# Kernel optimization log

Measured on AMD Instinct MI355X. Metric: run time of the kernel, lower is better.

The kernel has to match this reference:

```python
import jax, jax.numpy as jnp
import numpy as np

N, E, G, F = 100000, 3200000, 256, 15
NEG_SLOPE = 0.2


def _lin(k, fi, fo):
    s = 1.0 / np.sqrt(fi)
    return jax.random.uniform(k, (fi, fo), jnp.float32, -s, s)


def _vec(k, n, fi):
    s = 1.0 / np.sqrt(fi)
    return jax.random.uniform(k, (n,), jnp.float32, -s, s)


def setup_inputs() -> dict:
    key = jax.random.key(0)
    ks = jax.random.split(key, 40)
    inp = {}
    inp["x"] = jax.random.normal(ks[0], (N, F), jnp.float32)
    inp["edge_index"] = jax.random.randint(ks[1], (2, E), 0, N, dtype=jnp.int32)
    inp["batch"] = jnp.sort(jax.random.randint(ks[2], (N,), 0, G, dtype=jnp.int32))
    inp["xA"] = jax.random.normal(ks[3], (G, 300), jnp.float32)
    i = 4
    for l in (1, 2, 3):
        inp[f"cW{l}"] = _lin(ks[i], F, F); i += 1
        inp[f"cas{l}"] = _vec(ks[i], F, F); i += 1
        inp[f"cad{l}"] = _vec(ks[i], F, F); i += 1
        inp[f"cb{l}"] = jnp.zeros((F,), jnp.float32)
        inp[f"fW{l}"] = _lin(ks[i], F, F); i += 1
        inp[f"fb{l}"] = _vec(ks[i], F, F); i += 1
    inp["m1W"] = _lin(ks[i], 90, 90); i += 1
    inp["m1b"] = _vec(ks[i], 90, 90); i += 1
    inp["aW1"] = _lin(ks[i], 300, 300); i += 1
    inp["ab1"] = _vec(ks[i], 300, 300); i += 1
    inp["aW2"] = _lin(ks[i], 300, 300); i += 1
    inp["ab2"] = _vec(ks[i], 300, 300); i += 1
    inp["aW3"] = _lin(ks[i], 300, 300); i += 1
    inp["ab3"] = _vec(ks[i], 300, 300); i += 1
    inp["aW4"] = _lin(ks[i], 300, 45); i += 1
    inp["ab4"] = _vec(ks[i], 45, 300); i += 1
    inp["m2W"] = _lin(ks[i], 90, 1); i += 1
    inp["m2b"] = _vec(ks[i], 1, 90); i += 1
    return inp


def _gat(x, src, dst, W, a_s, a_d, b):
    """PyG GATConv (heads=1, add_self_loops handled by caller via src/dst)."""
    h = x @ W                                        # [N, F]
    e = jax.nn.leaky_relu((h @ a_s)[src] + (h @ a_d)[dst], NEG_SLOPE)  # [E+N]
    mx = jax.ops.segment_max(e, dst, num_segments=N)
    ex = jnp.exp(e - mx[dst])
    den = jax.ops.segment_sum(ex, dst, num_segments=N)
    alpha = ex / (den[dst] + 1e-16)                   # segment softmax over dst
    out = jax.ops.segment_sum(h[src] * alpha[:, None], dst, num_segments=N)
    return out + b


def reference(x, edge_index, batch, xA,
              cW1, cas1, cad1, cb1, fW1, fb1,
              cW2, cas2, cad2, cb2, fW2, fb2,
              cW3, cas3, cad3, cb3, fW3, fb3,
              m1W, m1b, aW1, ab1, aW2, ab2, aW3, ab3, aW4, ab4,
              m2W, m2b):
    loop = jnp.arange(N, dtype=edge_index.dtype)      # self loops
    src = jnp.concatenate([edge_index[0], loop])
    dst = jnp.concatenate([edge_index[1], loop])

    h = _gat(x, src, dst, cW1, cas1, cad1, cb1)
    h = jax.nn.relu(h @ fW1 + fb1)
    h = _gat(h, src, dst, cW2, cas2, cad2, cb2)
    h = jax.nn.relu(h @ fW2 + fb2)
    h = _gat(h, src, dst, cW3, cas3, cad3, cb3)
    h = h @ fW3 + fb3

    s = jax.ops.segment_sum(h, batch, num_segments=G)
    mx = jax.ops.segment_max(h, batch, num_segments=G)
    cnt = jax.ops.segment_sum(jnp.ones((N, 1), h.dtype), batch, num_segments=G)
    mean = s / jnp.maximum(cnt, 1.0)
    pooled = jnp.concatenate([s, mx, mean], axis=1)   # [G, 45]

    a = jax.nn.relu(xA @ aW1 + ab1)
    a = jax.nn.relu(a @ aW2 + ab2)
    a = jax.nn.sigmoid(a @ aW3 + ab3)
    xann = a @ aW4 + ab4                              # [G, 45]

    z = jnp.concatenate([pooled, xann], axis=1)       # [G, 90]
    z = jax.nn.relu(z @ m1W + m1b)
    z = z @ m2W + m2b
    return jax.nn.sigmoid(z)
```

## Files before the change

### kernel.cpp

```cpp
#include <hip/hip_runtime.h>
#include <hip/hip_bf16.h>
#include <math.h>

#define FDIM 15
#define FPAD 16
#define NEG_SLOPE 0.2f
#define BSH 8
#define BWID 256
#define HB_GRID 256
#define HB_BLK 1024

typedef _Float16 half_t;

__device__ __forceinline__ float leaky(float e) {
  return fmaxf(NEG_SLOPE * e, e);
}

__global__ void k_zero(int* __restrict__ p, int n) {
  int i = blockIdx.x * blockDim.x + threadIdx.x;
  if (i < n) p[i] = 0;
}

__global__ void k_bhist(const int* __restrict__ dstI, int* __restrict__ bcnt,
                        int n_tot, int n_real, int NB) {
  __shared__ int hist[512];
  int tid = threadIdx.x;
  for (int i = tid; i < NB; i += blockDim.x) hist[i] = 0;
  __syncthreads();
  int stride = gridDim.x * blockDim.x;
  for (int i = blockIdx.x * blockDim.x + tid; i < n_tot; i += stride) {
    int d = (i < n_real) ? dstI[i] : (i - n_real);
    atomicAdd(&hist[d >> BSH], 1);
  }
  __syncthreads();
  for (int i = tid; i < NB; i += blockDim.x)
    if (hist[i]) atomicAdd(&bcnt[i], hist[i]);
}

__global__ void k_bscan(const int* __restrict__ bcnt, int* __restrict__ boff,
                        int* __restrict__ bcur, int* __restrict__ rowptr,
                        int NB, int N, int total) {
  __shared__ int s[512];
  int tid = threadIdx.x;
  int v = (tid < NB) ? bcnt[tid] : 0;
  s[tid] = v;
  __syncthreads();
  for (int off = 1; off < 512; off <<= 1) {
    int add = (tid >= off) ? s[tid - off] : 0;
    __syncthreads();
    s[tid] += add;
    __syncthreads();
  }
  if (tid < NB) { int e = s[tid] - v; boff[tid] = e; bcur[tid] = e; }
  if (tid == NB - 1) boff[NB] = s[tid];
  if (tid == 0) rowptr[N] = total;
}

__global__ void k_bpart(const int* __restrict__ srcI, const int* __restrict__ dstI,
                        int* __restrict__ bcur, int* __restrict__ bbuf,
                        int n_tot, int n_real, int NB) {
  __shared__ int hist[512];
  __shared__ int base[512];
  int tid = threadIdx.x;
  for (int i = tid; i < NB; i += blockDim.x) hist[i] = 0;
  __syncthreads();
  int stride = gridDim.x * blockDim.x;
  int g0 = blockIdx.x * blockDim.x + tid;
  for (int i = g0; i < n_tot; i += stride) {
    int d = (i < n_real) ? dstI[i] : (i - n_real);
    atomicAdd(&hist[d >> BSH], 1);
  }
  __syncthreads();
  for (int i = tid; i < NB; i += blockDim.x)
    base[i] = hist[i] ? atomicAdd(&bcur[i], hist[i]) : 0;
  __syncthreads();
  for (int i = tid; i < NB; i += blockDim.x) hist[i] = 0;
  __syncthreads();
  for (int i = g0; i < n_tot; i += stride) {
    int s, d;
    if (i < n_real) { s = srcI[i]; d = dstI[i]; }
    else { s = d = i - n_real; }
    int b = d >> BSH;
    int p = base[b] + atomicAdd(&hist[b], 1);
    bbuf[p] = (s << BSH) | (d & (BWID - 1));
  }
}

__global__ void k_bbuild(const int* __restrict__ boff, const int* __restrict__ bbuf,
                         int* __restrict__ rowptr, int* __restrict__ csr, int N) {
  __shared__ int hist[BWID];
  __shared__ int sc[BWID];
  int b = blockIdx.x;
  int tid = threadIdx.x;
  int base_dst = b << BSH;
  int nd = min(BWID, N - base_dst);
  int s0 = boff[b], s1 = boff[b + 1];
  if (tid < BWID) hist[tid] = 0;
  __syncthreads();
  for (int j = s0 + tid; j < s1; j += 512)
    atomicAdd(&hist[bbuf[j] & (BWID - 1)], 1);
  __syncthreads();
  int v = 0;
  if (tid < BWID) { v = hist[tid]; sc[tid] = v; }
  __syncthreads();
  for (int off = 1; off < BWID; off <<= 1) {
    int add = 0;
    if (tid < BWID && tid >= off) add = sc[tid - off];
    __syncthreads();
    if (tid < BWID) sc[tid] += add;
    __syncthreads();
  }
  if (tid < nd) rowptr[base_dst + tid] = s0 + sc[tid] - v;
  __syncthreads();
  if (tid < BWID) hist[tid] = sc[tid] - v;
  __syncthreads();
  for (int j = s0 + tid; j < s1; j += 512) {
    int e = bbuf[j];
    int dl = e & (BWID - 1);
    int p = s0 + atomicAdd(&hist[dl], 1);
    csr[p] = (e >> BSH) << 5;
  }
}

__global__ void k_transform(const float* __restrict__ in, int ld_in,
                            const float* __restrict__ W,
                            const float* __restrict__ a_s,
                            const float* __restrict__ a_d,
                            half_t* __restrict__ hp,
                            float* __restrict__ ad_,
                            int n_nodes) {
  __shared__ float Ws[FDIM * FDIM];
  __shared__ float asv[FDIM], adv[FDIM];
  int tid = threadIdx.x;
  if (tid < FDIM * FDIM) Ws[tid] = W[tid];
  if (tid < FDIM) { asv[tid] = a_s[tid]; adv[tid] = a_d[tid]; }
  __syncthreads();
  int n = blockIdx.x * blockDim.x + tid;
  if (n >= n_nodes) return;
  float xin[FDIM];
#pragma unroll
  for (int j = 0; j < FDIM; ++j) xin[j] = in[n * ld_in + j];
  float sa = 0.f, da = 0.f;
  half_t hrow[FPAD];
#pragma unroll
  for (int o = 0; o < FDIM; ++o) {
    float acc = 0.f;
#pragma unroll
    for (int k = 0; k < FDIM; ++k) acc += xin[k] * Ws[k * FDIM + o];
    hrow[o] = (half_t)acc;
    sa += acc * asv[o];
    da += acc * adv[o];
  }
  hrow[FDIM] = (half_t)sa;
  ad_[n] = da;
  float4 w0, w1;
  __builtin_memcpy(&w0, &hrow[0], 16);
  __builtin_memcpy(&w1, &hrow[8], 16);
  float4* dst = (float4*)(hp + (size_t)n * FPAD);
  dst[0] = w0;
  dst[1] = w1;
}

__device__ __forceinline__ void mlp_rider(int g, int tid, int nthreads,
                                          const float* __restrict__ mIn,
                                          const float* __restrict__ mW,
                                          const float* __restrict__ mB,
                                          float* __restrict__ mOut,
                                          int Nout, int mAct,
                                          float* mins) {
  for (int k = tid; k < 300; k += nthreads) mins[k] = mIn[(size_t)g * 300 + k];
  __syncthreads();
  int j1 = tid;
  int j2 = tid + nthreads;
  bool p1 = (j1 < Nout), p2 = (j2 < Nout);
  if (!p1) return;
  float a0 = 0.f, a1 = 0.f, a2 = 0.f, a3 = 0.f;
  float a4 = 0.f, a5 = 0.f, a6 = 0.f, a7 = 0.f;
  float b0 = 0.f, b1 = 0.f, b2 = 0.f, b3 = 0.f;
  float b4 = 0.f, b5 = 0.f, b6 = 0.f, b7 = 0.f;
  int k = 0;
  for (; k + 7 < 300; k += 8) {
    float i0 = mins[k],     i1 = mins[k + 1], i2 = mins[k + 2], i3 = mins[k + 3];
    float i4 = mins[k + 4], i5 = mins[k + 5], i6 = mins[k + 6], i7 = mins[k + 7];
    float w0 = mW[k * Nout + j1];
    float w1 = mW[(k + 1) * Nout + j1];
    float w2 = mW[(k + 2) * Nout + j1];
    float w3 = mW[(k + 3) * Nout + j1];
    float w4 = mW[(k + 4) * Nout + j1];
    float w5 = mW[(k + 5) * Nout + j1];
    float w6 = mW[(k + 6) * Nout + j1];
    float w7 = mW[(k + 7) * Nout + j1];
    a0 += i0 * w0; a1 += i1 * w1; a2 += i2 * w2; a3 += i3 * w3;
    a4 += i4 * w4; a5 += i5 * w5; a6 += i6 * w6; a7 += i7 * w7;
    if (p2) {
      float v0 = mW[k * Nout + j2];
      float v1 = mW[(k + 1) * Nout + j2];
      float v2 = mW[(k + 2) * Nout + j2];
      float v3 = mW[(k + 3) * Nout + j2];
      float v4 = mW[(k + 4) * Nout + j2];
      float v5 = mW[(k + 5) * Nout + j2];
      float v6 = mW[(k + 6) * Nout + j2];
      float v7 = mW[(k + 7) * Nout + j2];
      b0 += i0 * v0; b1 += i1 * v1; b2 += i2 * v2; b3 += i3 * v3;
      b4 += i4 * v4; b5 += i5 * v5; b6 += i6 * v6; b7 += i7 * v7;
    }
  }
  for (; k < 300; ++k) {
    float ik = mins[k];
    a0 += ik * mW[k * Nout + j1];
    if (p2) b0 += ik * mW[k * Nout + j2];
  }
  float r1 = mB[j1] + ((a0 + a1) + (a2 + a3)) + ((a4 + a5) + (a6 + a7));
  if (mAct == 1) r1 = fmaxf(r1, 0.f);
  else if (mAct == 2) r1 = 1.f / (1.f + expf(-r1));
  mOut[(size_t)g * Nout + j1] = r1;
  if (p2) {
    float r2 = mB[j2] + ((b0 + b1) + (b2 + b3)) + ((b4 + b5) + (b6 + b7));
    if (mAct == 1) r2 = fmaxf(r2, 0.f);
    else if (mAct == 2) r2 = 1.f / (1.f + expf(-r2));
    mOut[(size_t)g * Nout + j2] = r2;
  }
}

__global__ void k_gat(const int* __restrict__ rowptr, const int* __restrict__ csrB,
                      const half_t* __restrict__ hp, const float* __restrict__ ad_,
                      const float* __restrict__ cb, const float* __restrict__ fW,
                      const float* __restrict__ fb,
                      const float* __restrict__ nW, const float* __restrict__ nas,
                      const float* __restrict__ nad,
                      half_t* __restrict__ hp2, float* __restrict__ ad2,
                      float* __restrict__ fout,
                      const float* __restrict__ mIn, const float* __restrict__ mW,
                      const float* __restrict__ mB, float* __restrict__ mOut,
                      int mNout, int mAct, int mlpG,
                      int n_nodes, int do_relu, int fuse) {
  __shared__ float Ws[FDIM * FDIM];
  __shared__ float W2s[FDIM * FDIM];
  __shared__ float cbv[FDIM], fbv[FDIM], as2v[FDIM], ad2v[FDIM];
  __shared__ float aggT[16][16];
  __shared__ float outT[16][16];
  __shared__ float mins[304];
  int tid = threadIdx.x;

  if ((int)blockIdx.x < mlpG) {
    mlp_rider(blockIdx.x, tid, blockDim.x, mIn, mW, mB, mOut, mNout, mAct, mins);
    return;
  }

  if (tid < FDIM * FDIM) Ws[tid] = fW[tid];
  if (tid < FDIM) { cbv[tid] = cb[tid]; fbv[tid] = fb[tid]; }
  if (fuse) {
    if (tid < FDIM * FDIM) W2s[tid] = nW[tid];
    if (tid < FDIM) { as2v[tid] = nas[tid]; ad2v[tid] = nad[tid]; }
  }
  __syncthreads();
  int dl = tid >> 4;
  int f  = tid & 15;
  int e4 = f >> 2;
  int c  = f & 3;
  int d  = ((int)blockIdx.x - mlpG) * 16 + dl;
  float r0 = 0.f, r1 = 0.f, r2 = 0.f, r3 = 0.f;
  if (d < n_nodes) {
    int rs = rowptr[d], re = rowptr[d + 1];
    float adv = ad_[d];
    const char* hb = (const char*)hp;
    int co = c << 3;
    int srcl = f | 3;
    float acc0 = 0.f, acc1 = 0.f, acc2 = 0.f, acc3 = 0.f, den = 0.f;
    for (int j = rs; j < re; j += 8) {
      int i0 = j + e4;
      int i1 = i0 + 4;
      int o0 = csrB[i0 < re ? i0 : re - 1];
      int o1 = csrB[i1 < re ? i1 : re - 1];
      uint2 u0 = *(const uint2*)(hb + o0 + co);
      uint2 u1 = *(const uint2*)(hb + o1 + co);
      half_t h0[4], h1[4];
      __builtin_memcpy(h0, &u0, 8);
      __builtin_memcpy(h1, &u1, 8);
      float a0 = (float)h0[0], a1 = (float)h0[1], a2 = (float)h0[2], a3 = (float)h0[3];
      float b0 = (float)h1[0], b1 = (float)h1[1], b2 = (float)h1[2], b3 = (float)h1[3];
      float s0 = __shfl(a3, srcl, 16);
      float s1 = __shfl(b3, srcl, 16);
      float w0 = (i0 < re) ? __expf(leaky(s0 + adv)) : 0.f;
      float w1 = (i1 < re) ? __expf(leaky(s1 + adv)) : 0.f;
      den  += w0 + w1;
      acc0 += a0 * w0 + b0 * w1;
      acc1 += a1 * w0 + b1 * w1;
      acc2 += a2 * w0 + b2 * w1;
      acc3 += a3 * w0 + b3 * w1;
    }
    den  += __shfl_xor(den,  4, 16);
    acc0 += __shfl_xor(acc0, 4, 16);
    acc1 += __shfl_xor(acc1, 4, 16);
    acc2 += __shfl_xor(acc2, 4, 16);
    acc3 += __shfl_xor(acc3, 4, 16);
    den  += __shfl_xor(den,  8, 16);
    acc0 += __shfl_xor(acc0, 8, 16);
    acc1 += __shfl_xor(acc1, 8, 16);
    acc2 += __shfl_xor(acc2, 8, 16);
    acc3 += __shfl_xor(acc3, 8, 16);
    float inv = 1.f / (den + 1e-16f);
    r0 = acc0 * inv; r1 = acc1 * inv; r2 = acc2 * inv; r3 = acc3 * inv;
  }
  if (e4 == 0) {
    int base = c << 2;
    aggT[dl][base]     = r0 + cbv[base];
    aggT[dl][base + 1] = r1 + cbv[base + 1];
    aggT[dl][base + 2] = r2 + cbv[base + 2];
    aggT[dl][base + 3] = (base + 3 < FDIM) ? (r3 + cbv[base + 3]) : 0.f;
  }
  __syncthreads();
  int o = f;
  float ffn = 0.f;
  if (o < FDIM) {
    ffn = fbv[o];
#pragma unroll
    for (int k = 0; k < FDIM; ++k) ffn += aggT[dl][k] * Ws[k * FDIM + o];
    if (do_relu) ffn = fmaxf(ffn, 0.f);
  }
  if (!fuse) {
    if (d < n_nodes) fout[d * FPAD + o] = (o < FDIM) ? ffn : 0.f;
    return;
  }
  outT[dl][o] = ffn;
  __syncthreads();
  if (d < n_nodes) {
    float h2 = 0.f;
    if (o < FDIM) {
#pragma unroll
      for (int k = 0; k < FDIM; ++k) h2 += outT[dl][k] * W2s[k * FDIM + o];
    }
    float pa = (o < FDIM) ? h2 * as2v[o] : 0.f;
    float pd = (o < FDIM) ? h2 * ad2v[o] : 0.f;
#pragma unroll
    for (int k = 8; k; k >>= 1) {
      pa += __shfl_xor(pa, k, 16);
      pd += __shfl_xor(pd, k, 16);
    }
    hp2[(size_t)d * FPAD + o] = (half_t)((o < FDIM) ? h2 : pa);
    if (o == 0) ad2[d] = pd;
  }
}

__device__ __forceinline__ int lowerb(const int* __restrict__ a, int n, int key) {
  int lo = 0, hi = n;
  while (lo < hi) { int mid = (lo + hi) >> 1; if (a[mid] < key) lo = mid + 1; else hi = mid; }
  return lo;
}

__global__ void k_pool(const float* __restrict__ fout, const int* __restrict__ batch,
                       float* __restrict__ pooled,
                       const float* __restrict__ acts,
                       const float* __restrict__ aW4, const float* __restrict__ ab4,
                       float* __restrict__ xann,
                       int n_nodes, int Gn) {
  __shared__ float ss[256], sm[256];
  __shared__ float mins[304];
  int tid = threadIdx.x;
  if ((int)blockIdx.x < Gn) {
    mlp_rider(blockIdx.x, tid, blockDim.x, acts, aW4, ab4, xann, 45, 0, mins);
    return;
  }
  int g = blockIdx.x - Gn;
  int s = lowerb(batch, n_nodes, g);
  int e = lowerb(batch, n_nodes, g + 1);
  int f = tid & 15;
  float sum = 0.f, mx = -INFINITY;
  for (int n = s + (tid >> 4); n < e; n += 16) {
    float v = fout[n * FPAD + f];
    sum += v;
    mx = fmaxf(mx, v);
  }
  ss[tid] = sum; sm[tid] = mx;
  __syncthreads();
  for (int step = 128; step >= 16; step >>= 1) {
    if (tid < step) { ss[tid] += ss[tid + step]; sm[tid] = fmaxf(sm[tid], sm[tid + step]); }
    __syncthreads();
  }
  if (tid < FDIM) {
    float cnt = (float)(e - s);
    float sv = ss[tid];
    pooled[g * 45 + tid] = sv;
    pooled[g * 45 + 15 + tid] = sm[tid];
    pooled[g * 45 + 30 + tid] = sv / fmaxf(cnt, 1.f);
  }
}

__global__ void k_final(const float* __restrict__ pooled, const float* __restrict__ xann,
                        const float* __restrict__ m1W, const float* __restrict__ m1b,
                        const float* __restrict__ m2W, const float* __restrict__ m2b,
                        float* __restrict__ out) {
  __shared__ float z[90];
  __shared__ float z2[90];
  __shared__ float ps[128];
  int g = blockIdx.x;
  int t = threadIdx.x;
  if (t < 45) z[t] = pooled[g * 45 + t];
  else if (t < 90) z[t] = xann[g * 45 + (t - 45)];
  __syncthreads();
  if (t < 90) {
    float a0 = 0.f, a1 = 0.f;
    for (int k = 0; k < 90; k += 2) {
      float w0 = m1W[k * 90 + t];
      float w1 = m1W[(k + 1) * 90 + t];
      a0 += z[k] * w0; a1 += z[k + 1] * w1;
    }
    z2[t] = fmaxf(m1b[t] + a0 + a1, 0.f);
  }
  __syncthreads();
  if (t < 90) ps[t] = z2[t] * m2W[t];
  else ps[t] = 0.f;
  __syncthreads();
  if (t < 64) {
    float v = ps[t] + ps[t + 64];
#pragma unroll
    for (int k2 = 32; k2; k2 >>= 1) v += __shfl_xor(v, k2, 64);
    if (t == 0) out[g] = 1.f / (1.f + expf(-(v + m2b[0])));
  }
}

extern "C" void kernel_launch(void* const* d_in, const int* in_sizes, int n_in,
                              void* d_out, int out_size, void* d_ws, size_t ws_size,
                              hipStream_t stream) {
  const float* x   = (const float*)d_in[0];
  const int* ei    = (const int*)d_in[1];
  const int* batch = (const int*)d_in[2];
  const float* xA  = (const float*)d_in[3];

  const int N = in_sizes[0] / FDIM;
  const int E = in_sizes[1] / 2;
  const int G = in_sizes[3] / 300;
  const int ET = E + N;
  const int NB = (N + BWID - 1) >> BSH;

  const int* srcI = ei;
  const int* dstI = ei + E;

  float* ws = (float*)d_ws;
  size_t layerW = (size_t)34 * N;
  size_t uSize = layerW > (size_t)ET ? layerW : (size_t)ET;
  size_t off = 0;
  int*    bbuf = (int*)(ws + off);
  half_t* hpA  = (half_t*)(ws + off);
  half_t* hpB  = (half_t*)(ws + off + (size_t)8 * N);
  float*  adA  = ws + off + (size_t)16 * N;
  float*  adB  = ws + off + (size_t)17 * N;
  float*  fout = ws + off + (size_t)18 * N;
  off += uSize;
  int*   rowptr = (int*)(ws + off); off += N + 1;
  int*   csr    = (int*)(ws + off); off += (size_t)ET;
  int*   bcnt   = (int*)(ws + off); off += 516;
  int*   boff   = (int*)(ws + off); off += 516;
  int*   bcur   = (int*)(ws + off); off += 516;
  float* pooled = ws + off; off += (size_t)G * 45;
  float* a1     = ws + off; off += (size_t)G * 300;
  float* a2     = ws + off; off += (size_t)G * 300;
  float* xann   = ws + off; off += (size_t)G * 45;

  const int B = 256;
  const int gN = (N + B - 1) / B;

  k_zero<<<(NB + B - 1) / B, B, 0, stream>>>(bcnt, NB);
  k_bhist<<<HB_GRID, HB_BLK, 0, stream>>>(dstI, bcnt, ET, E, NB);
  k_bscan<<<1, 512, 0, stream>>>(bcnt, boff, bcur, rowptr, NB, N, ET);
  k_bpart<<<HB_GRID, HB_BLK, 0, stream>>>(srcI, dstI, bcur, bbuf, ET, E, NB);
  k_bbuild<<<NB, 512, 0, stream>>>(boff, bbuf, rowptr, csr, N);

  const float* cW1  = (const float*)d_in[4];
  const float* cas1 = (const float*)d_in[5];
  const float* cad1 = (const float*)d_in[6];
  const float* cb1  = (const float*)d_in[7];
  const float* fW1  = (const float*)d_in[8];
  const float* fb1  = (const float*)d_in[9];
  const float* cW2  = (const float*)d_in[10];
  const float* cas2 = (const float*)d_in[11];
  const float* cad2 = (const float*)d_in[12];
  const float* cb2  = (const float*)d_in[13];
  const float* fW2  = (const float*)d_in[14];
  const float* fb2  = (const float*)d_in[15];
  const float* cW3  = (const float*)d_in[16];
  const float* cas3 = (const float*)d_in[17];
  const float* cad3 = (const float*)d_in[18];
  const float* cb3  = (const float*)d_in[19];
  const float* fW3  = (const float*)d_in[20];
  const float* fb3  = (const float*)d_in[21];
  const float* m1W  = (const float*)d_in[22];
  const float* m1b  = (const float*)d_in[23];
  const float* aW1  = (const float*)d_in[24];
  const float* ab1  = (const float*)d_in[25];
  const float* aW2  = (const float*)d_in[26];
  const float* ab2  = (const float*)d_in[27];
  const float* aW3  = (const float*)d_in[28];
  const float* ab3  = (const float*)d_in[29];
  const float* aW4  = (const float*)d_in[30];
  const float* ab4  = (const float*)d_in[31];
  const float* m2W  = (const float*)d_in[32];
  const float* m2b  = (const float*)d_in[33];

  const int gGat = (N + 15) / 16;
  k_transform<<<gN, B, 0, stream>>>(x, FDIM, cW1, cas1, cad1, hpA, adA, N);
  k_gat<<<gGat + G, B, 0, stream>>>(rowptr, csr, hpA, adA, cb1, fW1, fb1,
                                    cW2, cas2, cad2, hpB, adB, nullptr,
                                    xA, aW1, ab1, a1, 300, 1, G,
                                    N, 1, 1);
  k_gat<<<gGat + G, B, 0, stream>>>(rowptr, csr, hpB, adB, cb2, fW2, fb2,
                                    cW3, cas3, cad3, hpA, adA, nullptr,
                                    a1, aW2, ab2, a2, 300, 1, G,
                                    N, 1, 1);
  k_gat<<<gGat + G, B, 0, stream>>>(rowptr, csr, hpA, adA, cb3, fW3, fb3,
                                    nullptr, nullptr, nullptr, nullptr, nullptr, fout,
                                    a2, aW3, ab3, a1, 300, 2, G,
                                    N, 0, 0);

  k_pool<<<2 * G, B, 0, stream>>>(fout, batch, pooled, a1, aW4, ab4, xann, N, G);

  k_final<<<G, 128, 0, stream>>>(pooled, xann, m1W, m1b, m2W, m2b, (float*)d_out);
}
```

Before: 335.1 us.

## Software-pipeline CSR gather loop with 16-edge steps and prefetched indices

```diff
diff --git a/kernel.cpp b/kernel.cpp
--- a/kernel.cpp
+++ b/kernel.cpp
@@ -262,33 +262,64 @@
   float r0 = 0.f, r1 = 0.f, r2 = 0.f, r3 = 0.f;
   if (d < n_nodes) {
     int rs = rowptr[d], re = rowptr[d + 1];
+    int rlast = re - 1;
     float adv = ad_[d];
     const char* hb = (const char*)hp;
     int co = c << 3;
     int srcl = f | 3;
     float acc0 = 0.f, acc1 = 0.f, acc2 = 0.f, acc3 = 0.f, den = 0.f;
-    for (int j = rs; j < re; j += 8) {
-      int i0 = j + e4;
-      int i1 = i0 + 4;
-      int o0 = csrB[i0 < re ? i0 : re - 1];
-      int o1 = csrB[i1 < re ? i1 : re - 1];
-      uint2 u0 = *(const uint2*)(hb + o0 + co);
-      uint2 u1 = *(const uint2*)(hb + o1 + co);
-      half_t h0[4], h1[4];
-      __builtin_memcpy(h0, &u0, 8);
-      __builtin_memcpy(h1, &u1, 8);
-      float a0 = (float)h0[0], a1 = (float)h0[1], a2 = (float)h0[2], a3 = (float)h0[3];
-      float b0 = (float)h1[0], b1 = (float)h1[1], b2 = (float)h1[2], b3 = (float)h1[3];
+
+#define CLOAD(base, q0, q1, q2, q3)                              \
+    {                                                            \
+      int t0 = (base) + e4, t1 = t0 + 4, t2 = t0 + 8, t3 = t0 + 12; \
+      q0 = csrB[t0 < re ? t0 : rlast];                           \
+      q1 = csrB[t1 < re ? t1 : rlast];                           \
+      q2 = csrB[t2 < re ? t2 : rlast];                           \
+      q3 = csrB[t3 < re ? t3 : rlast];                           \
+    }
+
+    int oA0, oA1, oA2, oA3, oB0, oB1, oB2, oB3;
+    CLOAD(rs, oA0, oA1, oA2, oA3);
+    uint2 uA0 = *(const uint2*)(hb + oA0 + co);
+    uint2 uA1 = *(const uint2*)(hb + oA1 + co);
+    uint2 uA2 = *(const uint2*)(hb + oA2 + co);
+    uint2 uA3 = *(const uint2*)(hb + oA3 + co);
+    CLOAD(rs + 16, oB0, oB1, oB2, oB3);
+
+    for (int j = rs; j < re; j += 16) {
+      uint2 uB0 = *(const uint2*)(hb + oB0 + co);
+      uint2 uB1 = *(const uint2*)(hb + oB1 + co);
+      uint2 uB2 = *(const uint2*)(hb + oB2 + co);
+      uint2 uB3 = *(const uint2*)(hb + oB3 + co);
+      int oC0, oC1, oC2, oC3;
+      CLOAD(j + 32, oC0, oC1, oC2, oC3);
+      half_t ea[4], eb[4], ec[4], ed[4];
+      __builtin_memcpy(ea, &uA0, 8);
+      __builtin_memcpy(eb, &uA1, 8);
+      __builtin_memcpy(ec, &uA2, 8);
+      __builtin_memcpy(ed, &uA3, 8);
+      float a0 = (float)ea[0], a1 = (float)ea[1], a2 = (float)ea[2], a3 = (float)ea[3];
+      float b0 = (float)eb[0], b1 = (float)eb[1], b2 = (float)eb[2], b3 = (float)eb[3];
+      float p0 = (float)ec[0], p1 = (float)ec[1], p2 = (float)ec[2], p3 = (float)ec[3];
+      float q0 = (float)ed[0], q1 = (float)ed[1], q2 = (float)ed[2], q3 = (float)ed[3];
       float s0 = __shfl(a3, srcl, 16);
       float s1 = __shfl(b3, srcl, 16);
-      float w0 = (i0 < re) ? __expf(leaky(s0 + adv)) : 0.f;
-      float w1 = (i1 < re) ? __expf(leaky(s1 + adv)) : 0.f;
-      den  += w0 + w1;
-      acc0 += a0 * w0 + b0 * w1;
-      acc1 += a1 * w0 + b1 * w1;
-      acc2 += a2 * w0 + b2 * w1;
-      acc3 += a3 * w0 + b3 * w1;
+      float s2 = __shfl(p3, srcl, 16);
+      float s3 = __shfl(q3, srcl, 16);
+      int i0 = j + e4;
+      float w0 = (i0      < re) ? __expf(leaky(s0 + adv)) : 0.f;
+      float w1 = (i0 + 4  < re) ? __expf(leaky(s1 + adv)) : 0.f;
+      float w2 = (i0 + 8  < re) ? __expf(leaky(s2 + adv)) : 0.f;
+      float w3 = (i0 + 12 < re) ? __expf(leaky(s3 + adv)) : 0.f;
+      den  += (w0 + w1) + (w2 + w3);
+      acc0 += a0 * w0 + b0 * w1 + p0 * w2 + q0 * w3;
+      acc1 += a1 * w0 + b1 * w1 + p1 * w2 + q1 * w3;
+      acc2 += a2 * w0 + b2 * w1 + p2 * w2 + q2 * w3;
+      acc3 += a3 * w0 + b3 * w1 + p3 * w2 + q3 * w3;
+      uA0 = uB0; uA1 = uB1; uA2 = uB2; uA3 = uB3;
+      oB0 = oC0; oB1 = oC1; oB2 = oC2; oB3 = oC3;
     }
+#undef CLOAD
     den  += __shfl_xor(den,  4, 16);
     acc0 += __shfl_xor(acc0, 4, 16);
     acc1 += __shfl_xor(acc1, 4, 16);
```

Measured after the change: 323.7 us. 3.4% less time.
